# Performance work log

Hardware: AMD Instinct MI355X
Metric: run time of the kernel (lower is better)

Reference implementation:

```python
import jax, jax.numpy as jnp
import numpy as np

N = 100000
E = 1600000
C_IN = 128
C_OUT = 128
EPS = 1e-5


def setup_inputs() -> dict:
    key = jax.random.key(0)
    ks = jax.random.split(key, 8)
    x = jax.random.normal(ks[0], (N, C_IN), dtype=jnp.float32)
    edge_index = jax.random.randint(ks[1], (2, E), 0, N, dtype=jnp.int64)
    s_proj = 1.0 / np.sqrt(C_IN)
    s_out = 1.0 / np.sqrt(C_IN)
    W_proj = jax.random.uniform(ks[2], (C_IN, C_IN), jnp.float32, -s_proj, s_proj)
    b_proj = jax.random.uniform(ks[3], (C_IN,), jnp.float32, -s_proj, s_proj)
    W_l = jax.random.uniform(ks[4], (C_OUT, C_IN), jnp.float32, -s_out, s_out)
    b_l = jax.random.uniform(ks[5], (C_OUT,), jnp.float32, -s_out, s_out)
    W_r = jax.random.uniform(ks[6], (C_OUT, C_IN), jnp.float32, -s_out, s_out)
    gamma = jnp.ones((C_OUT,), jnp.float32)
    beta = jnp.zeros((C_OUT,), jnp.float32)
    return {"x": x, "edge_index": edge_index, "W_proj": W_proj, "b_proj": b_proj,
            "W_l": W_l, "b_l": b_l, "W_r": W_r, "gamma": gamma, "beta": beta}


def reference(x, edge_index, W_proj, b_proj, W_l, b_l, W_r, gamma, beta):
    # SAGEConv(project=True, aggr='sum'): project+ReLU source features per node,
    # gather along edges, scatter-sum at targets, then lin_l(agg) + lin_r(x_root).
    src, dst = edge_index[0], edge_index[1]
    h = jax.nn.relu(x @ W_proj.T + b_proj)            # [N, C_IN]
    msg = h[src]                                       # [E, C_IN] edge gather
    agg = jax.ops.segment_sum(msg, dst, num_segments=N)  # [N, C_IN]
    out = agg @ W_l.T + b_l + x @ W_r.T                # [N, C_OUT] (root uses unprojected x)
    # LayerNorm(c_out)
    mu = jnp.mean(out, axis=-1, keepdims=True)
    var = jnp.var(out, axis=-1, keepdims=True)
    return (out - mu) * jax.lax.rsqrt(var + EPS) * gamma + beta
```

## Files before the change

### kernel.cpp

```cpp
#include <hip/hip_runtime.h>
#include <stdint.h>

#define NN 100000
#define NE 1600000
#define C  128
#define NB 782
#define CAP 4096
#define SB_SHIFT 13
#define MBF 391
#define P1B 125
#define MBO 782

typedef __attribute__((ext_vector_type(8))) short short8;
typedef __attribute__((ext_vector_type(4))) float f32x4;

__device__ __forceinline__ float bf2f(uint16_t u) {
  union { uint32_t u; float f; } v; v.u = ((uint32_t)u) << 16; return v.f;
}
__device__ __forceinline__ uint16_t f2bf(float f) {
  union { float f; uint32_t u; } v; v.f = f;
  uint32_t r = v.u + 0x7fffu + ((v.u >> 16) & 1u);
  return (uint16_t)(r >> 16);
}
__device__ __forceinline__ float2 bf2x2(uint32_t u) {
  return make_float2(bf2f((uint16_t)u), bf2f((uint16_t)(u >> 16)));
}

__global__ __launch_bounds__(256) void cast3_k(
    const float* __restrict__ a, const float* __restrict__ b, const float* __restrict__ c,
    uint16_t* __restrict__ oa, uint16_t* __restrict__ ob, uint16_t* __restrict__ oc)
{
  int i = blockIdx.x * 256 + threadIdx.x;
  int which = i >> 12, j = i & 4095;
  const float* s = which == 0 ? a : (which == 1 ? b : c);
  uint16_t* d    = which == 0 ? oa : (which == 1 ? ob : oc);
  float4 v = ((const float4*)s)[j];
  uint2 p;
  p.x = (uint32_t)f2bf(v.x) | ((uint32_t)f2bf(v.y) << 16);
  p.y = (uint32_t)f2bf(v.z) | ((uint32_t)f2bf(v.w) << 16);
  ((uint2*)d)[j] = p;
}


__global__ __launch_bounds__(1024) void fused_front_k(
    const float* __restrict__ x, const uint16_t* __restrict__ wpb,
    const uint16_t* __restrict__ wrb,
    const float* __restrict__ bp, const float* __restrict__ bl,
    uint16_t* __restrict__ h, uint16_t* __restrict__ rb,
    const int* __restrict__ esrc, const int* __restrict__ edst,
    int* __restrict__ gcnt, uint32_t* __restrict__ ebuf)
{
  extern __shared__ uint8_t slds[];
  const int t = threadIdx.x;

  if (blockIdx.x < MBF) {
#pragma unroll
    for (int qq = 0; qq < 2; ++qq) {
      int ci = qq * 1024 + t;
      int c = ci >> 4, k16 = ci & 15;
      int slot = (k16 ^ (c & 15)) << 4;
      *(short8*)(slds + c * 256 + slot)         = *(const short8*)(wpb + ci * 8);
      *(short8*)(slds + 32768 + c * 256 + slot) = *(const short8*)(wrb + ci * 8);
    }
    __syncthreads();

    const int w = t >> 6, lane = t & 63;
    const int tile_m = blockIdx.x * 256 + w * 16;
    if (tile_m >= NN) return;
    const int r16 = lane & 15, g = lane >> 4;

    const int row = tile_m + r16;
    int arow = row < NN ? row : NN - 1;
    short8 a[4];
    const float* xp = x + (size_t)arow * C + g * 8;
#pragma unroll
    for (int kk = 0; kk < 4; ++kk) {
      float4 u = *(const float4*)(xp + kk * 32);
      float4 v = *(const float4*)(xp + kk * 32 + 4);
      short8 av;
      av[0] = (short)f2bf(u.x); av[1] = (short)f2bf(u.y);
      av[2] = (short)f2bf(u.z); av[3] = (short)f2bf(u.w);
      av[4] = (short)f2bf(v.x); av[5] = (short)f2bf(v.y);
      av[6] = (short)f2bf(v.z); av[7] = (short)f2bf(v.w);
      a[kk] = av;
    }

#pragma unroll
    for (int nt = 0; nt < 8; ++nt) {
      f32x4 hp = {0.f, 0.f, 0.f, 0.f};
      f32x4 hr = {0.f, 0.f, 0.f, 0.f};
      const int c = nt * 16 + r16;
      const uint8_t* rbp = slds + c * 256;
      const uint8_t* rbr = slds + 32768 + c * 256;
#pragma unroll
      for (int kk = 0; kk < 4; ++kk) {
        int slot = (((kk << 2) + g) ^ (c & 15)) << 4;
        hp = __builtin_amdgcn_mfma_f32_16x16x32_bf16(*(const short8*)(rbp + slot), a[kk], hp, 0, 0, 0);
        hr = __builtin_amdgcn_mfma_f32_16x16x32_bf16(*(const short8*)(rbr + slot), a[kk], hr, 0, 0, 0);
      }
      const int col0 = nt * 16 + g * 4;
      float4 bp4 = *(const float4*)(bp + col0);
      float4 bl4 = *(const float4*)(bl + col0);
      if (row < NN) {
        float h0 = hp[0] + bp4.x, h1 = hp[1] + bp4.y, h2 = hp[2] + bp4.z, h3 = hp[3] + bp4.w;
        h0 = h0 > 0.f ? h0 : 0.f; h1 = h1 > 0.f ? h1 : 0.f;
        h2 = h2 > 0.f ? h2 : 0.f; h3 = h3 > 0.f ? h3 : 0.f;
        uint2 ph;
        ph.x = (uint32_t)f2bf(h0) | ((uint32_t)f2bf(h1) << 16);
        ph.y = (uint32_t)f2bf(h2) | ((uint32_t)f2bf(h3) << 16);
        *(uint2*)(h + (size_t)row * C + col0) = ph;
        uint2 pr;
        pr.x = (uint32_t)f2bf(hr[0] + bl4.x) | ((uint32_t)f2bf(hr[1] + bl4.y) << 16);
        pr.y = (uint32_t)f2bf(hr[2] + bl4.z) | ((uint32_t)f2bf(hr[3] + bl4.w) << 16);
        *(uint2*)(rb + (size_t)row * C + col0) = pr;
      }
    }
  } else {
    int* bh = (int*)slds;
    int* gb = bh + NB;
    const int blk = blockIdx.x - MBF;
    const int base = blk * 12800;

    for (int i = t; i < NB; i += 1024) bh[i] = 0;

    const int4* ed4 = (const int4*)(edst + base);
    const int4* es4 = (const int4*)(esrc + base);
    int4 dv[4], sv[4];
    bool val[4];
#pragma unroll
    for (int k = 0; k < 4; ++k) {
      int i = t + k * 1024;
      val[k] = (i < 3200);
      if (val[k]) { dv[k] = ed4[i]; sv[k] = es4[i]; }
    }
    __syncthreads();

#pragma unroll
    for (int k = 0; k < 4; ++k) if (val[k]) {
      atomicAdd(&bh[dv[k].x >> 7], 1); atomicAdd(&bh[dv[k].y >> 7], 1);
      atomicAdd(&bh[dv[k].z >> 7], 1); atomicAdd(&bh[dv[k].w >> 7], 1);
    }
    __syncthreads();

    for (int i = t; i < NB; i += 1024) {
      int c = bh[i];
      gb[i] = c ? atomicAdd(&gcnt[i], c) : 0;
      bh[i] = 0;
    }
    __syncthreads();

#define P1_SCATTER(d, s) do { \
      int bb = (d) >> 7; \
      int o = atomicAdd(&bh[bb], 1); \
      int pos = gb[bb] + o; \
      if (pos < CAP) ebuf[(size_t)bb * CAP + pos] = ((uint32_t)((d) & 127) << 17) | (uint32_t)(s); \
    } while (0)

#pragma unroll
    for (int k = 0; k < 4; ++k) if (val[k]) {
      P1_SCATTER(dv[k].x, sv[k].x); P1_SCATTER(dv[k].y, sv[k].y);
      P1_SCATTER(dv[k].z, sv[k].z); P1_SCATTER(dv[k].w, sv[k].w);
    }
#undef P1_SCATTER
  }
}

__global__ __launch_bounds__(256) void phase2_k(
    const uint32_t* __restrict__ ebuf, const int* __restrict__ gcnt,
    int* __restrict__ ssrc, int2* __restrict__ sdeg)
{
  __shared__ uint32_t raw[CAP];
  __shared__ int lout[CAP];
  __shared__ int cnt2[128 * 16];
  __shared__ int nd[128];
  __shared__ int psum[256];
  const int b = blockIdx.x, t = threadIdx.x;
  const int n0 = b * 128;

  int acc = 0;
  for (int i = t; i < b; i += 256) acc += gcnt[i];
  psum[t] = acc;
  __syncthreads();
  for (int off = 128; off > 0; off >>= 1) {
    if (t < off) psum[t] += psum[t + off];
    __syncthreads();
  }
  const int base = psum[0];
  int cnt = gcnt[b]; if (cnt > CAP) cnt = CAP;

  for (int i = t; i < 128 * 16; i += 256) cnt2[i] = 0;
  __syncthreads();
  for (int i = t; i < cnt; i += 256) {
    uint32_t v = ebuf[(size_t)b * CAP + i];
    raw[i] = v;
    atomicAdd(&cnt2[(v >> 17) * 16 + ((v & 0x1FFFFu) >> SB_SHIFT)], 1);
  }
  __syncthreads();

  int deg_t = 0;
  if (t < 128) {
#pragma unroll
    for (int i = 0; i < 16; ++i) deg_t += cnt2[t * 16 + i];
    nd[t] = deg_t;
  }
  __syncthreads();
  for (int off = 1; off < 128; off <<= 1) {
    int v = 0;
    if (t < 128 && t >= off) v = nd[t - off];
    __syncthreads();
    if (t < 128) nd[t] += v;
    __syncthreads();
  }
  if (t < 128) {
    int pref = nd[t] - deg_t;
    if (n0 + t < NN) sdeg[n0 + t] = make_int2(base + pref, deg_t);
    int run = pref;
#pragma unroll
    for (int i = 0; i < 16; ++i) { int c = cnt2[t * 16 + i]; cnt2[t * 16 + i] = run; run += c; }
  }
  __syncthreads();
  for (int i = t; i < cnt; i += 256) {
    uint32_t v = raw[i];
    int o = atomicAdd(&cnt2[(v >> 17) * 16 + ((v & 0x1FFFFu) >> SB_SHIFT)], 1);
    lout[o] = (int)(v & 0x1FFFFu);
  }
  __syncthreads();
  for (int i = t; i < cnt; i += 256) ssrc[base + i] = lout[i];
}

__global__ __launch_bounds__(256) void aggregate_k(
    const uint16_t* __restrict__ h, const int* __restrict__ ssrc,
    const int2* __restrict__ sdeg, uint16_t* __restrict__ agg)
{
  const int wid = (blockIdx.x * 256 + threadIdx.x) >> 6;
  if (wid >= NN) return;
  const int lane = threadIdx.x & 63;
  const int q = lane >> 4;
  const int l16 = lane & 15;
  const int2 sd = sdeg[wid];
  const int s0 = sd.x, cnt = sd.y;
  const size_t choff = (size_t)l16 * 8;
  float2 a0 = {0.f, 0.f}, a1 = {0.f, 0.f}, a2 = {0.f, 0.f}, a3 = {0.f, 0.f};

#define ACC8(v) do { \
    a0 += bf2x2((v).x); a1 += bf2x2((v).y); \
    a2 += bf2x2((v).z); a3 += bf2x2((v).w); \
  } while (0)

  if (cnt > 0) {
    int e0 = ssrc[s0 + ((q      < cnt) ? q      : cnt - 1)];
    int e1 = ssrc[s0 + ((q + 4  < cnt) ? q + 4  : cnt - 1)];
    int e2 = ssrc[s0 + ((q + 8  < cnt) ? q + 8  : cnt - 1)];
    int e3 = ssrc[s0 + ((q + 12 < cnt) ? q + 12 : cnt - 1)];
    for (int j = 0; j < cnt; j += 16) {
      uint4 v0 = *(const uint4*)(h + (size_t)e0 * C + choff);
      uint4 v1 = *(const uint4*)(h + (size_t)e1 * C + choff);
      uint4 v2 = *(const uint4*)(h + (size_t)e2 * C + choff);
      uint4 v3 = *(const uint4*)(h + (size_t)e3 * C + choff);
      const int jn = j + 16;
      if (jn < cnt) {
        e0 = ssrc[s0 + ((jn + q      < cnt) ? jn + q      : cnt - 1)];
        e1 = ssrc[s0 + ((jn + q + 4  < cnt) ? jn + q + 4  : cnt - 1)];
        e2 = ssrc[s0 + ((jn + q + 8  < cnt) ? jn + q + 8  : cnt - 1)];
        e3 = ssrc[s0 + ((jn + q + 12 < cnt) ? jn + q + 12 : cnt - 1)];
      }
      if (j + q      < cnt) ACC8(v0);
      if (j + q + 4  < cnt) ACC8(v1);
      if (j + q + 8  < cnt) ACC8(v2);
      if (j + q + 12 < cnt) ACC8(v3);
    }
  }
#undef ACC8

#pragma unroll
  for (int msk = 16; msk <= 32; msk <<= 1) {
    a0.x += __shfl_xor(a0.x, msk, 64); a0.y += __shfl_xor(a0.y, msk, 64);
    a1.x += __shfl_xor(a1.x, msk, 64); a1.y += __shfl_xor(a1.y, msk, 64);
    a2.x += __shfl_xor(a2.x, msk, 64); a2.y += __shfl_xor(a2.y, msk, 64);
    a3.x += __shfl_xor(a3.x, msk, 64); a3.y += __shfl_xor(a3.y, msk, 64);
  }
  if (q == 0) {
    uint4 p;
    p.x = (uint32_t)f2bf(a0.x) | ((uint32_t)f2bf(a0.y) << 16);
    p.y = (uint32_t)f2bf(a1.x) | ((uint32_t)f2bf(a1.y) << 16);
    p.z = (uint32_t)f2bf(a2.x) | ((uint32_t)f2bf(a2.y) << 16);
    p.w = (uint32_t)f2bf(a3.x) | ((uint32_t)f2bf(a3.y) << 16);
    *(uint4*)(agg + (size_t)wid * C + choff) = p;
  }
}

__global__ __launch_bounds__(512) void gemm_out_k(
    const uint16_t* __restrict__ aggb, const uint16_t* __restrict__ rb,
    const uint16_t* __restrict__ wlb, const float* __restrict__ gamma,
    const float* __restrict__ beta, float* __restrict__ out)
{
  __shared__ uint8_t wl[32768];
  const int t = threadIdx.x;
#pragma unroll
  for (int qq = 0; qq < 4; ++qq) {
    int ci = qq * 512 + t;
    int c = ci >> 4, k16 = ci & 15;
    *(short8*)(wl + c * 256 + ((k16 ^ (c & 15)) << 4)) = *(const short8*)(wlb + ci * 8);
  }
  __syncthreads();

  const int w = t >> 6, lane = t & 63;
  const int tile_m = blockIdx.x * 128 + w * 16;
  if (tile_m >= NN) return;
  const int r16 = lane & 15, g = lane >> 4;

  const int row = tile_m + r16;
  const int arow = row < NN ? row : NN - 1;
  short8 a0[4];
  const uint16_t* p0 = aggb + (size_t)arow * C + g * 8;
#pragma unroll
  for (int kk = 0; kk < 4; ++kk) a0[kk] = *(const short8*)(p0 + kk * 32);

  f32x4 acc[8];
  float s1 = 0.f, s2 = 0.f;
#pragma unroll
  for (int nt = 0; nt < 8; ++nt) {
    f32x4 c4 = {0.f, 0.f, 0.f, 0.f};
    const int c = nt * 16 + r16;
    const uint8_t* rbl = wl + c * 256;
#pragma unroll
    for (int kk = 0; kk < 4; ++kk) {
      short8 b = *(const short8*)(rbl + ((((kk << 2) + g) ^ (c & 15)) << 4));
      c4 = __builtin_amdgcn_mfma_f32_16x16x32_bf16(b, a0[kk], c4, 0, 0, 0);
    }
    const int col0 = nt * 16 + g * 4;
    uint2 rv = *(const uint2*)(rb + (size_t)arow * C + col0);
    float2 r01 = bf2x2(rv.x), r23 = bf2x2(rv.y);
    c4[0] += r01.x; c4[1] += r01.y; c4[2] += r23.x; c4[3] += r23.y;
#pragma unroll
    for (int rr = 0; rr < 4; ++rr) { s1 += c4[rr]; s2 += c4[rr] * c4[rr]; }
    acc[nt] = c4;
  }

  s1 += __shfl_xor(s1, 16, 64); s2 += __shfl_xor(s2, 16, 64);
  s1 += __shfl_xor(s1, 32, 64); s2 += __shfl_xor(s2, 32, 64);
  const float mean = s1 * (1.f / C);
  const float var = s2 * (1.f / C) - mean * mean;
  const float rstd = rsqrtf(var + 1e-5f);

  if (row < NN) {
#pragma unroll
    for (int nt = 0; nt < 8; ++nt) {
      const int col0 = nt * 16 + g * 4;
      float4 gm = *(const float4*)(gamma + col0);
      float4 bt = *(const float4*)(beta + col0);
      float4 o;
      o.x = (acc[nt][0] - mean) * rstd * gm.x + bt.x;
      o.y = (acc[nt][1] - mean) * rstd * gm.y + bt.y;
      o.z = (acc[nt][2] - mean) * rstd * gm.z + bt.z;
      o.w = (acc[nt][3] - mean) * rstd * gm.w + bt.w;
      *(float4*)(out + (size_t)row * C + col0) = o;
    }
  }
}

extern "C" void kernel_launch(void* const* d_in, const int* in_sizes, int n_in,
                              void* d_out, int out_size, void* d_ws, size_t ws_size,
                              hipStream_t stream)
{
  const float* x        = (const float*)d_in[0];
  const int* ei         = (const int*)d_in[1];
  const float* Wp       = (const float*)d_in[2];
  const float* bp       = (const float*)d_in[3];
  const float* Wl       = (const float*)d_in[4];
  const float* bl       = (const float*)d_in[5];
  const float* Wr       = (const float*)d_in[6];
  const float* gamma    = (const float*)d_in[7];
  const float* beta     = (const float*)d_in[8];
  float* out            = (float*)d_out;

  char* ws = (char*)d_ws;
  uint16_t* rb   = (uint16_t*)(ws + 0);
  uint16_t* h    = (uint16_t*)(ws + 25600000);
  uint32_t* ebuf = (uint32_t*)(ws + 51200000);
  uint16_t* aggb = (uint16_t*)(ws + 51200000);
  uint16_t* wpb  = (uint16_t*)(ws + 76800000);
  uint16_t* wlb  = (uint16_t*)(ws + 76832768);
  uint16_t* wrb  = (uint16_t*)(ws + 76865536);
  int2* sdeg     = (int2*)(ws + 76898304);
  int* gcnt      = (int*)(ws + 77698304);
  int* ssrc      = (int*)(ws + 78102400);

  const int* esrc = ei;
  const int* edst = ei + NE;

  hipMemsetAsync(gcnt, 0, NB * sizeof(int), stream);

  cast3_k<<<48, 256, 0, stream>>>(Wp, Wl, Wr, wpb, wlb, wrb);

  fused_front_k<<<MBF + P1B, 1024, 65536, stream>>>(
      x, wpb, wrb, bp, bl, h, rb, esrc, edst, gcnt, ebuf);

  phase2_k<<<NB, 256, 0, stream>>>(ebuf, gcnt, ssrc, sdeg);

  aggregate_k<<<(NN + 3) / 4, 256, 0, stream>>>(h, ssrc, sdeg, aggb);

  gemm_out_k<<<MBO, 512, 0, stream>>>(aggb, rb, wlb, gamma, beta, out);
}
```

Measured before the change: 150.8 us.

## Split front GEMM into column halves with 512-thread blocks

The fused front kernel now runs 512-thread blocks. Each GEMM block covers 128 rows and one 64-column half of the projection and root weights, so every block loads only half of each weight matrix into 32 KB of LDS. The histogram/bucketing blocks are doubled in count and each handles half as many edges. The goal is more, smaller blocks with less LDS per block, for better occupancy and load balance. The cost is that each x row tile is read and converted twice, once per half.

```diff
diff --git a/kernel.cpp b/kernel.cpp
--- a/kernel.cpp
+++ b/kernel.cpp
@@ -7,8 +7,8 @@
 #define NB 782
 #define CAP 4096
 #define SB_SHIFT 13
-#define MBF 391
-#define P1B 125
+#define GEMMB 1564
+#define P1B 250
 #define MBO 782
 
 typedef __attribute__((ext_vector_type(8))) short short8;
@@ -42,7 +42,7 @@
 }
 
 
-__global__ __launch_bounds__(1024) void fused_front_k(
+__global__ __launch_bounds__(512) void fused_front_k(
     const float* __restrict__ x, const uint16_t* __restrict__ wpb,
     const uint16_t* __restrict__ wrb,
     const float* __restrict__ bp, const float* __restrict__ bl,
@@ -53,24 +53,28 @@
   extern __shared__ uint8_t slds[];
   const int t = threadIdx.x;
 
-  if (blockIdx.x < MBF) {
-#pragma unroll
-    for (int qq = 0; qq < 2; ++qq) {
-      int ci = qq * 1024 + t;
-      int c = ci >> 4, k16 = ci & 15;
-      int slot = (k16 ^ (c & 15)) << 4;
-      *(short8*)(slds + c * 256 + slot)         = *(const short8*)(wpb + ci * 8);
-      *(short8*)(slds + 32768 + c * 256 + slot) = *(const short8*)(wrb + ci * 8);
+  if (blockIdx.x < GEMMB) {
+    const int half  = blockIdx.x & 1;
+    const int rtile = blockIdx.x >> 1;
+#pragma unroll
+    for (int qq = 0; qq < 4; ++qq) {
+      int ci = qq * 512 + t;
+      int m  = ci >> 10;
+      int cj = ci & 1023;
+      int cl = cj >> 4, k16 = cj & 15;
+      const uint16_t* wsrc = m == 0 ? wpb : wrb;
+      *(short8*)(slds + m * 16384 + cl * 256 + ((k16 ^ (cl & 15)) << 4)) =
+          *(const short8*)(wsrc + ((size_t)(half * 64 + cl) * 16 + k16) * 8);
     }
     __syncthreads();
 
     const int w = t >> 6, lane = t & 63;
-    const int tile_m = blockIdx.x * 256 + w * 16;
+    const int tile_m = rtile * 128 + w * 16;
     if (tile_m >= NN) return;
     const int r16 = lane & 15, g = lane >> 4;
 
     const int row = tile_m + r16;
-    int arow = row < NN ? row : NN - 1;
+    const int arow = row < NN ? row : NN - 1;
     short8 a[4];
     const float* xp = x + (size_t)arow * C + g * 8;
 #pragma unroll
@@ -86,19 +90,19 @@
     }
 
 #pragma unroll
-    for (int nt = 0; nt < 8; ++nt) {
+    for (int nt = 0; nt < 4; ++nt) {
       f32x4 hp = {0.f, 0.f, 0.f, 0.f};
       f32x4 hr = {0.f, 0.f, 0.f, 0.f};
-      const int c = nt * 16 + r16;
-      const uint8_t* rbp = slds + c * 256;
-      const uint8_t* rbr = slds + 32768 + c * 256;
+      const int cl = nt * 16 + r16;
+      const uint8_t* rbp = slds + cl * 256;
+      const uint8_t* rbr = slds + 16384 + cl * 256;
 #pragma unroll
       for (int kk = 0; kk < 4; ++kk) {
-        int slot = (((kk << 2) + g) ^ (c & 15)) << 4;
+        int slot = (((kk << 2) + g) ^ (cl & 15)) << 4;
         hp = __builtin_amdgcn_mfma_f32_16x16x32_bf16(*(const short8*)(rbp + slot), a[kk], hp, 0, 0, 0);
         hr = __builtin_amdgcn_mfma_f32_16x16x32_bf16(*(const short8*)(rbr + slot), a[kk], hr, 0, 0, 0);
       }
-      const int col0 = nt * 16 + g * 4;
+      const int col0 = half * 64 + nt * 16 + g * 4;
       float4 bp4 = *(const float4*)(bp + col0);
       float4 bl4 = *(const float4*)(bl + col0);
       if (row < NN) {
@@ -118,10 +122,10 @@
   } else {
     int* bh = (int*)slds;
     int* gb = bh + NB;
-    const int blk = blockIdx.x - MBF;
-    const int base = blk * 12800;
-
-    for (int i = t; i < NB; i += 1024) bh[i] = 0;
+    const int blk = blockIdx.x - GEMMB;
+    const int base = blk * 6400;
+
+    for (int i = t; i < NB; i += 512) bh[i] = 0;
 
     const int4* ed4 = (const int4*)(edst + base);
     const int4* es4 = (const int4*)(esrc + base);
@@ -129,8 +133,8 @@
     bool val[4];
 #pragma unroll
     for (int k = 0; k < 4; ++k) {
-      int i = t + k * 1024;
-      val[k] = (i < 3200);
+      int i = t + k * 512;
+      val[k] = (i < 1600);
       if (val[k]) { dv[k] = ed4[i]; sv[k] = es4[i]; }
     }
     __syncthreads();
@@ -142,7 +146,7 @@
     }
     __syncthreads();
 
-    for (int i = t; i < NB; i += 1024) {
+    for (int i = t; i < NB; i += 512) {
       int c = bh[i];
       gb[i] = c ? atomicAdd(&gcnt[i], c) : 0;
       bh[i] = 0;
@@ -393,7 +397,7 @@
 
   cast3_k<<<48, 256, 0, stream>>>(Wp, Wl, Wr, wpb, wlb, wrb);
 
-  fused_front_k<<<MBF + P1B, 1024, 65536, stream>>>(
+  fused_front_k<<<GEMMB + P1B, 512, 32768, stream>>>(
       x, wpb, wrb, bp, bl, h, rb, esrc, edst, gcnt, ebuf);
 
   phase2_k<<<NB, 256, 0, stream>>>(ebuf, gcnt, ssrc, sdeg);
```

Measured after the change: 152.1 us. Within noise of the previous version (+0.9%).
